# Kernel optimization log

Measured on AMD Instinct MI355X. Metric: run time of the kernel, lower is better.

## Reference

```python
import jax, jax.numpy as jnp
import numpy as np

N_NODES = 100000


def _graph_conv(x, W, b, src, dst, norm_src, norm_dst):
    """DGL GraphConv with norm='both'. Transform-before-aggregate when
    in_feats > out_feats (true for both layers in this config)."""
    h = x * norm_src[:, None]          # D_out^{-1/2} * X
    if W.shape[0] > W.shape[1]:        # in > out: mult W first (cheaper aggregation)
        h = h @ W
        m = jax.ops.segment_sum(h[src], dst, num_segments=N_NODES)
    else:
        m = jax.ops.segment_sum(h[src], dst, num_segments=N_NODES)
        m = m @ W
    return m * norm_dst[:, None] + b   # D_in^{-1/2} * (...) + bias


def setup_inputs() -> dict:
    key = jax.random.key(0)
    k1, k2, k3, k4, k5 = jax.random.split(key, 5)
    in_feats, hidden, n_classes = 256, 64, 40
    n_edges = 1600000
    features = jax.random.normal(k1, (N_NODES, in_feats), dtype=jnp.float32)
    src = jax.random.randint(k2, (n_edges,), 0, N_NODES, dtype=jnp.int64)
    dst = jax.random.randint(k3, (n_edges,), 0, N_NODES, dtype=jnp.int64)
    W1 = jax.random.normal(k4, (in_feats, hidden), dtype=jnp.float32) * (1.0 / np.sqrt(in_feats))
    b1 = jnp.zeros((hidden,), dtype=jnp.float32)
    W2 = jax.random.normal(k5, (hidden, n_classes), dtype=jnp.float32) * (1.0 / np.sqrt(hidden))
    b2 = jnp.zeros((n_classes,), dtype=jnp.float32)
    return {"features": features, "src": src, "dst": dst,
            "W1": W1, "b1": b1, "W2": W2, "b2": b2}


def reference(features, src, dst, W1, b1, W2, b2):
    ones_e = jnp.ones(src.shape[0], dtype=features.dtype)
    out_deg = jax.ops.segment_sum(ones_e, src, num_segments=N_NODES)
    in_deg = jax.ops.segment_sum(ones_e, dst, num_segments=N_NODES)
    norm_src = jax.lax.rsqrt(jnp.maximum(out_deg, 1.0))
    norm_dst = jax.lax.rsqrt(jnp.maximum(in_deg, 1.0))

    h = _graph_conv(features, W1, b1, src, dst, norm_src, norm_dst)
    x = jax.nn.relu(h)
    x = _graph_conv(x, W2, b2, src, dst, norm_src, norm_dst)
    return (x, h)
```

## Files before the change

kernel.cpp:

```cpp
#include <hip/hip_runtime.h>
#include <hip/hip_bf16.h>

#define NN       100000
#define NE       1600000
#define IN_F     256
#define HID      64
#define NC       40
#define CAP      64
#define NBKT     391
#define NBP1     500
#define EPB      3200
#define EI4      800
#define NB_GEMM  1563

typedef __attribute__((ext_vector_type(8))) short bf16x8;
typedef __attribute__((ext_vector_type(4))) float f32x4;

__device__ __forceinline__ unsigned short f2bf(float x) {
    unsigned int u = __builtin_bit_cast(unsigned int, x);
    u += 0x7FFFu + ((u >> 16) & 1u);
    return (unsigned short)(u >> 16);
}
__device__ __forceinline__ float bf2f(unsigned short h) {
    unsigned int u = ((unsigned int)h) << 16;
    return __builtin_bit_cast(float, u);
}

__global__ __launch_bounds__(256) void k_count(const int* __restrict__ src,
                                               const int* __restrict__ dst,
                                               const float* __restrict__ W1,
                                               const float* __restrict__ W2,
                                               unsigned short* __restrict__ Bp,
                                               unsigned short* __restrict__ Bp2,
                                               int* __restrict__ gcnt) {
    __shared__ int sh[2 * NBKT];
    const int cb = blockIdx.x, t = threadIdx.x;
    if (cb >= NBP1 + 8) {
        const int tid = (cb - NBP1 - 8) * 256 + t;
        if (tid >= 6 * 64) return;
        const int lane = tid & 63, f = tid >> 6;
        const int nt = f % 3, kt = f / 3;
        const int col = nt * 16 + (lane & 15);
        const int kb  = kt * 32 + (lane >> 4) * 8;
        unsigned short o[8];
        #pragma unroll
        for (int j = 0; j < 8; ++j)
            o[j] = (col < NC) ? f2bf(W2[(kb + j) * NC + col]) : (unsigned short)0;
        #pragma unroll
        for (int j = 0; j < 8; ++j) Bp2[tid * 8 + j] = o[j];
        return;
    }
    if (cb >= NBP1) {
        const int tid = (cb - NBP1) * 256 + t;
        const int lane = tid & 63, nt = (tid >> 6) & 3, kt = tid >> 8;
        const int col = nt * 16 + (lane & 15);
        const int kb  = kt * 32 + (lane >> 4) * 8;
        unsigned short o[8];
        #pragma unroll
        for (int j = 0; j < 8; ++j) o[j] = f2bf(W1[(kb + j) * HID + col]);
        #pragma unroll
        for (int j = 0; j < 8; ++j) Bp[tid * 8 + j] = o[j];
        return;
    }
    for (int j = t; j < 2 * NBKT; j += 256) sh[j] = 0;
    __syncthreads();
    const int4* s4 = reinterpret_cast<const int4*>(src) + (size_t)cb * EI4;
    const int4* d4 = reinterpret_cast<const int4*>(dst) + (size_t)cb * EI4;
    for (int i = t; i < EI4; i += 256) {
        const int4 d = d4[i], s = s4[i];
        atomicAdd(&sh[d.x >> 8], 1);
        atomicAdd(&sh[d.y >> 8], 1);
        atomicAdd(&sh[d.z >> 8], 1);
        atomicAdd(&sh[d.w >> 8], 1);
        atomicAdd(&sh[NBKT + (s.x >> 8)], 1);
        atomicAdd(&sh[NBKT + (s.y >> 8)], 1);
        atomicAdd(&sh[NBKT + (s.z >> 8)], 1);
        atomicAdd(&sh[NBKT + (s.w >> 8)], 1);
    }
    __syncthreads();
    for (int k = t; k < 2 * NBKT; k += 256) gcnt[k * NBP1 + cb] = sh[k];
}

__global__ __launch_bounds__(256) void k_gemm1(const float* __restrict__ X,
                                               const unsigned short* __restrict__ Bp,
                                               const float* __restrict__ nsrcf,
                                               unsigned short* __restrict__ h1b) {
    __shared__ unsigned short xt[64 * 256];
    const int bid = blockIdx.x, t = threadIdx.x;
    const int r0 = bid * 64;

    f32x4 v[16];
    #pragma unroll
    for (int q = 0; q < 16; ++q) {
        const int idx = q * 1024 + t * 4;
        const int row = idx >> 8, col = idx & 255;
        const int gr  = (r0 + row < NN) ? (r0 + row) : (NN - 1);
        v[q] = *reinterpret_cast<const f32x4*>(X + (size_t)gr * IN_F + col);
    }
    __builtin_amdgcn_sched_barrier(0);
    #pragma unroll
    for (int q = 0; q < 16; ++q) {
        const int idx = q * 1024 + t * 4;
        const int row = idx >> 8, col = idx & 255;
        const unsigned int w0 = (unsigned)f2bf(v[q][0]) | ((unsigned)f2bf(v[q][1]) << 16);
        const unsigned int w1 = (unsigned)f2bf(v[q][2]) | ((unsigned)f2bf(v[q][3]) << 16);
        const int a = ((row * 256 + col) * 2) ^ ((row & 7) << 4);
        uint2 pk; pk.x = w0; pk.y = w1;
        *reinterpret_cast<uint2*>(reinterpret_cast<char*>(xt) + a) = pk;
    }
    __syncthreads();
    const int lane = t & 63;
    const int wid  = t >> 6;
    const int rloc = wid * 16 + (lane & 15);
    const bf16x8* bp = reinterpret_cast<const bf16x8*>(Bp) + lane;

    f32x4 acc0 = {0.f, 0.f, 0.f, 0.f};
    f32x4 acc1 = {0.f, 0.f, 0.f, 0.f};
    f32x4 acc2 = {0.f, 0.f, 0.f, 0.f};
    f32x4 acc3 = {0.f, 0.f, 0.f, 0.f};

    #pragma unroll
    for (int kt = 0; kt < 8; ++kt) {
        const int koff = (lane >> 4) * 8 + kt * 32;
        const int a = ((rloc * 256 + koff) * 2) ^ ((rloc & 7) << 4);
        const bf16x8 av = *reinterpret_cast<const bf16x8*>(
                              reinterpret_cast<char*>(xt) + a);
        const bf16x8 b0 = bp[(kt * 4 + 0) * 64];
        const bf16x8 b1 = bp[(kt * 4 + 1) * 64];
        const bf16x8 b2 = bp[(kt * 4 + 2) * 64];
        const bf16x8 b3 = bp[(kt * 4 + 3) * 64];
        acc0 = __builtin_amdgcn_mfma_f32_16x16x32_bf16(av, b0, acc0, 0, 0, 0);
        acc1 = __builtin_amdgcn_mfma_f32_16x16x32_bf16(av, b1, acc1, 0, 0, 0);
        acc2 = __builtin_amdgcn_mfma_f32_16x16x32_bf16(av, b2, acc2, 0, 0, 0);
        acc3 = __builtin_amdgcn_mfma_f32_16x16x32_bf16(av, b3, acc3, 0, 0, 0);
    }

    const int crow = r0 + wid * 16 + (lane >> 4) * 4;
    const int ccol = lane & 15;
    #pragma unroll
    for (int rr = 0; rr < 4; ++rr) {
        const int orow = crow + rr;
        if (orow < NN) {
            const float ns = nsrcf[orow];
            unsigned short* o = h1b + (size_t)orow * HID + ccol;
            o[0]  = f2bf(acc0[rr] * ns);
            o[16] = f2bf(acc1[rr] * ns);
            o[32] = f2bf(acc2[rr] * ns);
            o[48] = f2bf(acc3[rr] * ns);
        }
    }
}

__global__ __launch_bounds__(256) void k_scanA(const int* __restrict__ gcnt,
                                               int* __restrict__ bsum) {
    __shared__ int red[256];
    const int r = blockIdx.x, t = threadIdx.x;
    int x = gcnt[r * NBP1 + t];
    if (256 + t < NBP1) x += gcnt[r * NBP1 + 256 + t];
    red[t] = x;
    __syncthreads();
    for (int off = 128; off > 0; off >>= 1) {
        if (t < off) red[t] += red[t + off];
        __syncthreads();
    }
    if (t == 0) bsum[r] = red[0];
}

__global__ __launch_bounds__(512) void k_scanB(const int* __restrict__ bsum,
                                               int* __restrict__ bstart) {
    __shared__ int sa[512], sb[512];
    const int a = blockIdx.x, t = threadIdx.x;
    const int x = (t < NBKT) ? bsum[a * NBKT + t] : 0;
    sa[t] = x;
    __syncthreads();
    int* pin = sa; int* pout = sb;
    for (int off = 1; off < 512; off <<= 1) {
        int v = pin[t];
        if (t >= off) v += pin[t - off];
        pout[t] = v;
        __syncthreads();
        int* tmp = pin; pin = pout; pout = tmp;
    }
    if (t <= NBKT) bstart[a * (NBKT + 1) + t] = pin[t] - x;
}

__global__ __launch_bounds__(512) void k_scanC(int* __restrict__ gcnt,
                                               const int* __restrict__ bstart) {
    __shared__ int sa[512], sb[512];
    const int r = blockIdx.x, t = threadIdx.x;
    const int a = r / NBKT;
    const int x = (t < NBP1) ? gcnt[r * NBP1 + t] : 0;
    sa[t] = x;
    __syncthreads();
    int* pin = sa; int* pout = sb;
    for (int off = 1; off < 512; off <<= 1) {
        int v = pin[t];
        if (t >= off) v += pin[t - off];
        pout[t] = v;
        __syncthreads();
        int* tmp = pin; pin = pout; pout = tmp;
    }
    if (t < NBP1) gcnt[r * NBP1 + t] = bstart[r + a] + pin[t] - x;
}

__global__ __launch_bounds__(256) void k_scatter(const int* __restrict__ src,
                                                 const int* __restrict__ dst,
                                                 const int* __restrict__ gbase,
                                                 int* __restrict__ pedge,
                                                 unsigned char* __restrict__ psrc) {
    __shared__ int cur[2 * NBKT];
    const int b = blockIdx.x, t = threadIdx.x;
    for (int k = t; k < 2 * NBKT; k += 256) cur[k] = gbase[k * NBP1 + b];
    __syncthreads();
    const int4* s4 = reinterpret_cast<const int4*>(src) + (size_t)b * EI4;
    const int4* d4 = reinterpret_cast<const int4*>(dst) + (size_t)b * EI4;
    for (int i = t; i < EI4; i += 256) {
        const int4 dd = d4[i], ss = s4[i];
        {
            const int posD = atomicAdd(&cur[dd.x >> 8], 1);
            pedge[posD] = ss.x | ((dd.x & 255) << 17);
            const int posS = atomicAdd(&cur[NBKT + (ss.x >> 8)], 1);
            psrc[posS] = (unsigned char)(ss.x & 255);
        }
        {
            const int posD = atomicAdd(&cur[dd.y >> 8], 1);
            pedge[posD] = ss.y | ((dd.y & 255) << 17);
            const int posS = atomicAdd(&cur[NBKT + (ss.y >> 8)], 1);
            psrc[posS] = (unsigned char)(ss.y & 255);
        }
        {
            const int posD = atomicAdd(&cur[dd.z >> 8], 1);
            pedge[posD] = ss.z | ((dd.z & 255) << 17);
            const int posS = atomicAdd(&cur[NBKT + (ss.z >> 8)], 1);
            psrc[posS] = (unsigned char)(ss.z & 255);
        }
        {
            const int posD = atomicAdd(&cur[dd.w >> 8], 1);
            pedge[posD] = ss.w | ((dd.w & 255) << 17);
            const int posS = atomicAdd(&cur[NBKT + (ss.w >> 8)], 1);
            psrc[posS] = (unsigned char)(ss.w & 255);
        }
    }
}

__global__ __launch_bounds__(256) void k_place(const int* __restrict__ pedge,
                                               const unsigned char* __restrict__ psrc,
                                               const int* __restrict__ bstart,
                                               int* __restrict__ eidx,
                                               int* __restrict__ ideg,
                                               float* __restrict__ nsrcf) {
    __shared__ int cnt[256];
    const int kk = blockIdx.x, t = threadIdx.x;
    cnt[t] = 0;
    __syncthreads();
    if (kk < NBKT) {
        const int k  = kk;
        const int i0 = bstart[k], i1 = bstart[k + 1];
        for (int i = i0 + t; i < i1; i += 256) {
            const int v  = pedge[i];
            const int s  = v & 0x1FFFF;
            const int lo = v >> 17;
            const int c  = atomicAdd(&cnt[lo], 1);
            if (c < CAP) eidx[(size_t)((k << 8) | lo) * CAP + c] = s;
        }
        __syncthreads();
        const int d = (k << 8) | t;
        if (d < NN) ideg[d] = cnt[t];
    } else {
        const int k  = kk - NBKT;
        const int* bs = bstart + (NBKT + 1);
        const int i0 = bs[k], i1 = bs[k + 1];
        for (int i = i0 + t; i < i1; i += 256)
            atomicAdd(&cnt[psrc[i]], 1);
        __syncthreads();
        const int d = (k << 8) | t;
        if (d < NN) nsrcf[d] = rsqrtf(fmaxf((float)cnt[t], 1.f));
    }
}

__global__ __launch_bounds__(256) void k_agg64(const int* __restrict__ eidx,
                                               const int* __restrict__ ideg,
                                               const unsigned short* __restrict__ h1b,
                                               const float* __restrict__ b1,
                                               float* __restrict__ hout) {
    const int w    = (blockIdx.x * 256 + threadIdx.x) >> 6;
    const int lane = threadIdx.x & 63;
    if (w >= NN) return;
    const int cnt  = ideg[w];
    const int m    = cnt < CAP ? cnt : CAP;
    const int idxv = eidx[(size_t)w * CAP + lane];
    const int g    = lane >> 4;
    const unsigned fofs = (unsigned)(lane & 15) * 8u;
    const char* hb = reinterpret_cast<const char*>(h1b);
    float ax = 0.f, ay = 0.f, az = 0.f, aw = 0.f;

    #define G4_64(J0, OUT)                                                    \
        {                                                                     \
            const int s0 = __builtin_amdgcn_readlane(idxv, (J0));             \
            const int s1 = __builtin_amdgcn_readlane(idxv, (J0) + 1);         \
            const int s2 = __builtin_amdgcn_readlane(idxv, (J0) + 2);         \
            const int s3 = __builtin_amdgcn_readlane(idxv, (J0) + 3);         \
            const int slo = (lane & 16) ? s1 : s0;                            \
            const int shi = (lane & 16) ? s3 : s2;                            \
            const int s   = (lane & 32) ? shi : slo;                          \
            OUT = *reinterpret_cast<const uint2*>(hb + (unsigned)s * 128u + fofs); \
        }

    int j = 0;
    for (; j + 16 <= m; j += 16) {
        uint2 q0, q1, q2, q3;
        G4_64(j + 0,  q0); G4_64(j + 4,  q1); G4_64(j + 8,  q2); G4_64(j + 12, q3);
        ax += bf2f((unsigned short)(q0.x & 0xffffu)) + bf2f((unsigned short)(q1.x & 0xffffu))
            + bf2f((unsigned short)(q2.x & 0xffffu)) + bf2f((unsigned short)(q3.x & 0xffffu));
        ay += bf2f((unsigned short)(q0.x >> 16)) + bf2f((unsigned short)(q1.x >> 16))
            + bf2f((unsigned short)(q2.x >> 16)) + bf2f((unsigned short)(q3.x >> 16));
        az += bf2f((unsigned short)(q0.y & 0xffffu)) + bf2f((unsigned short)(q1.y & 0xffffu))
            + bf2f((unsigned short)(q2.y & 0xffffu)) + bf2f((unsigned short)(q3.y & 0xffffu));
        aw += bf2f((unsigned short)(q0.y >> 16)) + bf2f((unsigned short)(q1.y >> 16))
            + bf2f((unsigned short)(q2.y >> 16)) + bf2f((unsigned short)(q3.y >> 16));
    }
    for (; j < m; j += 4) {
        const int c1 = (j + 1 < m) ? j + 1 : m - 1;
        const int c2 = (j + 2 < m) ? j + 2 : m - 1;
        const int c3 = (j + 3 < m) ? j + 3 : m - 1;
        const int s0 = __builtin_amdgcn_readlane(idxv, j);
        const int s1 = __builtin_amdgcn_readlane(idxv, c1);
        const int s2 = __builtin_amdgcn_readlane(idxv, c2);
        const int s3 = __builtin_amdgcn_readlane(idxv, c3);
        const int slo = (lane & 16) ? s1 : s0;
        const int shi = (lane & 16) ? s3 : s2;
        const int s   = (lane & 32) ? shi : slo;
        const uint2 v = *reinterpret_cast<const uint2*>(hb + (unsigned)s * 128u + fofs);
        const float mk = (j + g < m) ? 1.f : 0.f;
        ax = fmaf(bf2f((unsigned short)(v.x & 0xffffu)), mk, ax);
        ay = fmaf(bf2f((unsigned short)(v.x >> 16)), mk, ay);
        az = fmaf(bf2f((unsigned short)(v.y & 0xffffu)), mk, az);
        aw = fmaf(bf2f((unsigned short)(v.y >> 16)), mk, aw);
    }
    #undef G4_64
    ax += __shfl(ax, lane ^ 16); ax += __shfl(ax, lane ^ 32);
    ay += __shfl(ay, lane ^ 16); ay += __shfl(ay, lane ^ 32);
    az += __shfl(az, lane ^ 16); az += __shfl(az, lane ^ 32);
    aw += __shfl(aw, lane ^ 16); aw += __shfl(aw, lane ^ 32);
    if (lane < 16) {
        const float nd = rsqrtf(fmaxf((float)cnt, 1.f));
        const f32x4 bb = *reinterpret_cast<const f32x4*>(b1 + lane * 4);
        f32x4 o;
        o[0] = fmaf(ax, nd, bb[0]);
        o[1] = fmaf(ay, nd, bb[1]);
        o[2] = fmaf(az, nd, bb[2]);
        o[3] = fmaf(aw, nd, bb[3]);
        *reinterpret_cast<f32x4*>(hout + (size_t)w * HID + lane * 4) = o;
    }
}

__global__ __launch_bounds__(256) void k_gemm2(const float* __restrict__ h,
                                               const unsigned short* __restrict__ Bp2,
                                               const float* __restrict__ nsrcf,
                                               unsigned short* __restrict__ xwb) {
    const int t = threadIdx.x;
    const int lane = t & 63;
    const int wid  = t >> 6;
    const int r0w  = blockIdx.x * 64 + wid * 16;
    if (r0w >= NN) return;
    const int row = r0w + (lane & 15);
    const float* hr = h + (size_t)row * HID + (lane >> 4) * 8;
    const bf16x8* bp = reinterpret_cast<const bf16x8*>(Bp2) + lane;

    f32x4 acc0 = {0.f, 0.f, 0.f, 0.f};
    f32x4 acc1 = {0.f, 0.f, 0.f, 0.f};
    f32x4 acc2 = {0.f, 0.f, 0.f, 0.f};
    #pragma unroll
    for (int kt = 0; kt < 2; ++kt) {
        const f32x4 v0 = *reinterpret_cast<const f32x4*>(hr + kt * 32);
        const f32x4 v1 = *reinterpret_cast<const f32x4*>(hr + kt * 32 + 4);
        bf16x8 a;
        a[0] = (short)f2bf(fmaxf(v0[0], 0.f));
        a[1] = (short)f2bf(fmaxf(v0[1], 0.f));
        a[2] = (short)f2bf(fmaxf(v0[2], 0.f));
        a[3] = (short)f2bf(fmaxf(v0[3], 0.f));
        a[4] = (short)f2bf(fmaxf(v1[0], 0.f));
        a[5] = (short)f2bf(fmaxf(v1[1], 0.f));
        a[6] = (short)f2bf(fmaxf(v1[2], 0.f));
        a[7] = (short)f2bf(fmaxf(v1[3], 0.f));
        const bf16x8 b0 = bp[(kt * 3 + 0) * 64];
        const bf16x8 b1 = bp[(kt * 3 + 1) * 64];
        const bf16x8 b2 = bp[(kt * 3 + 2) * 64];
        acc0 = __builtin_amdgcn_mfma_f32_16x16x32_bf16(a, b0, acc0, 0, 0, 0);
        acc1 = __builtin_amdgcn_mfma_f32_16x16x32_bf16(a, b1, acc1, 0, 0, 0);
        acc2 = __builtin_amdgcn_mfma_f32_16x16x32_bf16(a, b2, acc2, 0, 0, 0);
    }
    const int crow = r0w + (lane >> 4) * 4;
    const int ccol = lane & 15;
    #pragma unroll
    for (int rr = 0; rr < 4; ++rr) {
        const int orow = crow + rr;
        const float ns = nsrcf[orow];
        unsigned short* o = xwb + (size_t)orow * 64 + ccol;
        o[0]  = f2bf(acc0[rr] * ns);
        o[16] = f2bf(acc1[rr] * ns);
        o[32] = f2bf(acc2[rr] * ns);
        o[48] = 0;
    }
}

__global__ __launch_bounds__(256) void k_agg40(const int* __restrict__ eidx,
                                               const int* __restrict__ ideg,
                                               const unsigned short* __restrict__ xwb,
                                               const float* __restrict__ b2,
                                               float* __restrict__ out) {
    const int w    = (blockIdx.x * 256 + threadIdx.x) >> 6;
    const int lane = threadIdx.x & 63;
    if (w >= NN) return;
    const int cnt  = ideg[w];
    const int m    = cnt < CAP ? cnt : CAP;
    const int idxv = eidx[(size_t)w * CAP + lane];
    const int g    = lane >> 4;
    const unsigned fofs = (unsigned)(lane & 15) * 8u;
    const char* xb = reinterpret_cast<const char*>(xwb);
    float ax = 0.f, ay = 0.f, az = 0.f, aw = 0.f;

    #define G4_40(J0, OUT)                                                    \
        {                                                                     \
            const int s0 = __builtin_amdgcn_readlane(idxv, (J0));             \
            const int s1 = __builtin_amdgcn_readlane(idxv, (J0) + 1);         \
            const int s2 = __builtin_amdgcn_readlane(idxv, (J0) + 2);         \
            const int s3 = __builtin_amdgcn_readlane(idxv, (J0) + 3);         \
            const int slo = (lane & 16) ? s1 : s0;                            \
            const int shi = (lane & 16) ? s3 : s2;                            \
            const int s   = (lane & 32) ? shi : slo;                          \
            OUT = *reinterpret_cast<const uint2*>(xb + (unsigned)s * 128u + fofs); \
        }

    int j = 0;
    for (; j + 16 <= m; j += 16) {
        uint2 q0, q1, q2, q3;
        G4_40(j + 0,  q0); G4_40(j + 4,  q1); G4_40(j + 8,  q2); G4_40(j + 12, q3);
        ax += bf2f((unsigned short)(q0.x & 0xffffu)) + bf2f((unsigned short)(q1.x & 0xffffu))
            + bf2f((unsigned short)(q2.x & 0xffffu)) + bf2f((unsigned short)(q3.x & 0xffffu));
        ay += bf2f((unsigned short)(q0.x >> 16)) + bf2f((unsigned short)(q1.x >> 16))
            + bf2f((unsigned short)(q2.x >> 16)) + bf2f((unsigned short)(q3.x >> 16));
        az += bf2f((unsigned short)(q0.y & 0xffffu)) + bf2f((unsigned short)(q1.y & 0xffffu))
            + bf2f((unsigned short)(q2.y & 0xffffu)) + bf2f((unsigned short)(q3.y & 0xffffu));
        aw += bf2f((unsigned short)(q0.y >> 16)) + bf2f((unsigned short)(q1.y >> 16))
            + bf2f((unsigned short)(q2.y >> 16)) + bf2f((unsigned short)(q3.y >> 16));
    }
    for (; j < m; j += 4) {
        const int c1 = (j + 1 < m) ? j + 1 : m - 1;
        const int c2 = (j + 2 < m) ? j + 2 : m - 1;
        const int c3 = (j + 3 < m) ? j + 3 : m - 1;
        const int s0 = __builtin_amdgcn_readlane(idxv, j);
        const int s1 = __builtin_amdgcn_readlane(idxv, c1);
        const int s2 = __builtin_amdgcn_readlane(idxv, c2);
        const int s3 = __builtin_amdgcn_readlane(idxv, c3);
        const int slo = (lane & 16) ? s1 : s0;
        const int shi = (lane & 16) ? s3 : s2;
        const int s   = (lane & 32) ? shi : slo;
        const uint2 v = *reinterpret_cast<const uint2*>(xb + (unsigned)s * 128u + fofs);
        const float mk = (j + g < m) ? 1.f : 0.f;
        ax = fmaf(bf2f((unsigned short)(v.x & 0xffffu)), mk, ax);
        ay = fmaf(bf2f((unsigned short)(v.x >> 16)), mk, ay);
        az = fmaf(bf2f((unsigned short)(v.y & 0xffffu)), mk, az);
        aw = fmaf(bf2f((unsigned short)(v.y >> 16)), mk, aw);
    }
    #undef G4_40
    ax += __shfl(ax, lane ^ 16); ax += __shfl(ax, lane ^ 32);
    ay += __shfl(ay, lane ^ 16); ay += __shfl(ay, lane ^ 32);
    az += __shfl(az, lane ^ 16); az += __shfl(az, lane ^ 32);
    aw += __shfl(aw, lane ^ 16); aw += __shfl(aw, lane ^ 32);
    if (lane < 10) {
        const float nd = rsqrtf(fmaxf((float)cnt, 1.f));
        const f32x4 bb = *reinterpret_cast<const f32x4*>(b2 + lane * 4);
        f32x4 o;
        o[0] = fmaf(ax, nd, bb[0]);
        o[1] = fmaf(ay, nd, bb[1]);
        o[2] = fmaf(az, nd, bb[2]);
        o[3] = fmaf(aw, nd, bb[3]);
        *reinterpret_cast<f32x4*>(out + (size_t)w * NC + lane * 4) = o;
    }
}

extern "C" void kernel_launch(void* const* d_in, const int* in_sizes, int n_in,
                              void* d_out, int out_size, void* d_ws, size_t ws_size,
                              hipStream_t stream) {
    const float* X   = (const float*)d_in[0];
    const int*   src = (const int*)d_in[1];
    const int*   dst = (const int*)d_in[2];
    const float* W1  = (const float*)d_in[3];
    const float* b1  = (const float*)d_in[4];
    const float* W2  = (const float*)d_in[5];
    const float* b2  = (const float*)d_in[6];

    float* out  = (float*)d_out;
    float* xout = out;
    float* hout = out + (size_t)NN * NC;

    int* gcnt   = (int*)xout;
    int* bsum   = gcnt + 2 * NBKT * NBP1;
    int* bstart = bsum + 2 * NBKT;
    int* pedge  = (int*)hout;
    unsigned char* psrc = (unsigned char*)(pedge + NE);

    char* ws = (char*)d_ws;
    int* ideg  = (int*)ws;                            ws += sizeof(int) * NN;
    int* eidx  = (int*)ws;                            ws += sizeof(int) * (size_t)NN * CAP;
    unsigned short* Bp  = (unsigned short*)ws;        ws += sizeof(unsigned short) * 8 * 4 * 64 * 8;
    unsigned short* Bp2 = (unsigned short*)ws;        ws += sizeof(unsigned short) * 6 * 64 * 8;
    float* nsrcf = (float*)ws;                        ws += sizeof(float) * NN;
    unsigned short* h1b = (unsigned short*)ws;
    unsigned short* xwb = h1b;

    k_count  <<<NBP1 + 10, 256, 0, stream>>>(src, dst, W1, W2, Bp, Bp2, gcnt);
    k_scanA  <<<2 * NBKT, 256, 0, stream>>>(gcnt, bsum);
    k_scanB  <<<2, 512, 0, stream>>>(bsum, bstart);
    k_scanC  <<<2 * NBKT, 512, 0, stream>>>(gcnt, bstart);
    k_scatter<<<NBP1, 256, 0, stream>>>(src, dst, gcnt, pedge, psrc);
    k_place  <<<2 * NBKT, 256, 0, stream>>>(pedge, psrc, bstart, eidx, ideg, nsrcf);
    k_gemm1  <<<NB_GEMM, 256, 0, stream>>>(X, Bp, nsrcf, h1b);
    k_agg64  <<<(NN * 64 + 255) / 256, 256, 0, stream>>>(eidx, ideg, h1b, b1, hout);
    k_gemm2  <<<NB_GEMM, 256, 0, stream>>>(hout, Bp2, nsrcf, xwb);
    k_agg40  <<<(NN * 64 + 255) / 256, 256, 0, stream>>>(eidx, ideg, xwb, b2, xout);
}
```

Measured before the change: 173.6 us.

## Replace padded per-node edge slots with compact CSR row pointers

The per-destination edge index table changes from a fixed 64-slot padded array (NN*CAP ints) to a compact CSR layout with a row pointer array. k_place now counts in-degrees per bucket, runs a shared-memory prefix scan and places edges contiguously. The aggregation kernels read neighbor indices from the compact array starting at each node's row pointer. This cuts workspace footprint and the index-read traffic (about 25.6MB padded versus 6.4MB compact), and it drops the CAP truncation on placement. In exchange k_place makes an extra pass over the edges and does a block scan.

Measured after the change: 197.0 us. 1.14x slower.

```diff
diff --git a/kernel.cpp b/kernel.cpp
--- a/kernel.cpp
+++ b/kernel.cpp
@@ -246,26 +246,40 @@
 __global__ __launch_bounds__(256) void k_place(const int* __restrict__ pedge,
                                                const unsigned char* __restrict__ psrc,
                                                const int* __restrict__ bstart,
-                                               int* __restrict__ eidx,
+                                               int* __restrict__ eidxc,
+                                               int* __restrict__ rowptr,
                                                int* __restrict__ ideg,
                                                float* __restrict__ nsrcf) {
-    __shared__ int cnt[256];
+    __shared__ int cnt[256], sa[256], sb[256];
     const int kk = blockIdx.x, t = threadIdx.x;
     cnt[t] = 0;
     __syncthreads();
     if (kk < NBKT) {
-        const int k  = kk;
-        const int i0 = bstart[k], i1 = bstart[k + 1];
+        const int i0 = bstart[kk], i1 = bstart[kk + 1];
+        for (int i = i0 + t; i < i1; i += 256)
+            atomicAdd(&cnt[pedge[i] >> 17], 1);
+        __syncthreads();
+        sa[t] = cnt[t];
+        __syncthreads();
+        int* pin = sa; int* pout = sb;
+        for (int off = 1; off < 256; off <<= 1) {
+            int v = pin[t];
+            if (t >= off) v += pin[t - off];
+            pout[t] = v;
+            __syncthreads();
+            int* tmp = pin; pin = pout; pout = tmp;
+        }
+        const int base = i0 + pin[t] - cnt[t];
+        const int d = (kk << 8) | t;
+        if (d < NN) { rowptr[d] = base; ideg[d] = cnt[t]; }
+        __syncthreads();
+        cnt[t] = base;
+        __syncthreads();
         for (int i = i0 + t; i < i1; i += 256) {
-            const int v  = pedge[i];
-            const int s  = v & 0x1FFFF;
-            const int lo = v >> 17;
-            const int c  = atomicAdd(&cnt[lo], 1);
-            if (c < CAP) eidx[(size_t)((k << 8) | lo) * CAP + c] = s;
-        }
-        __syncthreads();
-        const int d = (k << 8) | t;
-        if (d < NN) ideg[d] = cnt[t];
+            const int v = pedge[i];
+            const int c = atomicAdd(&cnt[v >> 17], 1);
+            eidxc[c] = v & 0x1FFFF;
+        }
     } else {
         const int k  = kk - NBKT;
         const int* bs = bstart + (NBKT + 1);
@@ -278,7 +292,8 @@
     }
 }
 
-__global__ __launch_bounds__(256) void k_agg64(const int* __restrict__ eidx,
+__global__ __launch_bounds__(256) void k_agg64(const int* __restrict__ eidxc,
+                                               const int* __restrict__ rowptr,
                                                const int* __restrict__ ideg,
                                                const unsigned short* __restrict__ h1b,
                                                const float* __restrict__ b1,
@@ -288,7 +303,9 @@
     if (w >= NN) return;
     const int cnt  = ideg[w];
     const int m    = cnt < CAP ? cnt : CAP;
-    const int idxv = eidx[(size_t)w * CAP + lane];
+    const int i0   = rowptr[w];
+    const int ia   = i0 + lane;
+    const int idxv = eidxc[ia < NE ? ia : NE - 1];
     const int g    = lane >> 4;
     const unsigned fofs = (unsigned)(lane & 15) * 8u;
     const char* hb = reinterpret_cast<const char*>(h1b);
@@ -404,7 +421,8 @@
     }
 }
 
-__global__ __launch_bounds__(256) void k_agg40(const int* __restrict__ eidx,
+__global__ __launch_bounds__(256) void k_agg40(const int* __restrict__ eidxc,
+                                               const int* __restrict__ rowptr,
                                                const int* __restrict__ ideg,
                                                const unsigned short* __restrict__ xwb,
                                                const float* __restrict__ b2,
@@ -414,7 +432,9 @@
     if (w >= NN) return;
     const int cnt  = ideg[w];
     const int m    = cnt < CAP ? cnt : CAP;
-    const int idxv = eidx[(size_t)w * CAP + lane];
+    const int i0   = rowptr[w];
+    const int ia   = i0 + lane;
+    const int idxv = eidxc[ia < NE ? ia : NE - 1];
     const int g    = lane >> 4;
     const unsigned fofs = (unsigned)(lane & 15) * 8u;
     const char* xb = reinterpret_cast<const char*>(xwb);
@@ -502,8 +522,9 @@
     unsigned char* psrc = (unsigned char*)(pedge + NE);
 
     char* ws = (char*)d_ws;
-    int* ideg  = (int*)ws;                            ws += sizeof(int) * NN;
-    int* eidx  = (int*)ws;                            ws += sizeof(int) * (size_t)NN * CAP;
+    int* ideg   = (int*)ws;                           ws += sizeof(int) * NN;
+    int* rowptr = (int*)ws;                           ws += sizeof(int) * (NN + 16);
+    int* eidxc  = (int*)ws;                           ws += sizeof(int) * (size_t)NE;
     unsigned short* Bp  = (unsigned short*)ws;        ws += sizeof(unsigned short) * 8 * 4 * 64 * 8;
     unsigned short* Bp2 = (unsigned short*)ws;        ws += sizeof(unsigned short) * 6 * 64 * 8;
     float* nsrcf = (float*)ws;                        ws += sizeof(float) * NN;
@@ -515,9 +536,9 @@
     k_scanB  <<<2, 512, 0, stream>>>(bsum, bstart);
     k_scanC  <<<2 * NBKT, 512, 0, stream>>>(gcnt, bstart);
     k_scatter<<<NBP1, 256, 0, stream>>>(src, dst, gcnt, pedge, psrc);
-    k_place  <<<2 * NBKT, 256, 0, stream>>>(pedge, psrc, bstart, eidx, ideg, nsrcf);
+    k_place  <<<2 * NBKT, 256, 0, stream>>>(pedge, psrc, bstart, eidxc, rowptr, ideg, nsrcf);
     k_gemm1  <<<NB_GEMM, 256, 0, stream>>>(X, Bp, nsrcf, h1b);
-    k_agg64  <<<(NN * 64 + 255) / 256, 256, 0, stream>>>(eidx, ideg, h1b, b1, hout);
+    k_agg64  <<<(NN * 64 + 255) / 256, 256, 0, stream>>>(eidxc, rowptr, ideg, h1b, b1, hout);
     k_gemm2  <<<NB_GEMM, 256, 0, stream>>>(hout, Bp2, nsrcf, xwb);
-    k_agg40  <<<(NN * 64 + 255) / 256, 256, 0, stream>>>(eidx, ideg, xwb, b2, xout);
-}
+    k_agg40  <<<(NN * 64 + 255) / 256, 256, 0, stream>>>(eidxc, rowptr, ideg, xwb, b2, xout);
+}
```
